# Kernel optimization log

Measured on AMD Instinct MI355X. Metric: run time of the kernel, lower is better.

The kernel has to match this reference:

```python
import jax, jax.numpy as jnp
import numpy as np

B, L, C = 2, 8192, 256
K, NLEV = 17, 4
HALF = K // 2


def setup_inputs() -> dict:
    key = jax.random.key(0)
    ks = jax.random.split(key, 10)
    s = 0.02
    return {
        "x": jax.random.normal(ks[0], (B, L, C), jnp.float32),
        "stem_w": jax.random.normal(ks[1], (C, C, 2), jnp.float32) * s,   # Conv1d (out,in,k)
        "stem_b": jax.random.normal(ks[2], (C,), jnp.float32) * s,
        "qkv_w": jax.random.normal(ks[3], (3 * C, C), jnp.float32) * s,
        "width_w": jax.random.normal(ks[4], (1, C), jnp.float32) * s,
        "width_b": jax.random.normal(ks[5], (1,), jnp.float32) * s,
        "out_w": jax.random.normal(ks[6], (C, C), jnp.float32) * s,
        "query": jax.random.normal(ks[7], (NLEV * C,), jnp.float32) * s,
        "film_w": jax.random.normal(ks[8], (2 * C, NLEV * C), jnp.float32) * s,
        "film_b": jax.random.normal(ks[9], (2 * C,), jnp.float32) * s,
    }


def _local_attn(h, qkv_w, width_w, width_b, out_w):
    # h: (b, l, c); 1D local windowed attention with learned sigmoid distance mask
    b, l, c = h.shape
    rel_dist = jnp.abs(jnp.arange(K, dtype=h.dtype) - HALF)  # (K,)
    max_dist = float(HALF)
    scale = c ** -0.5
    qkv = h @ qkv_w.T
    q, k, v = jnp.split(qkv, 3, axis=-1)
    width = jax.nn.sigmoid(h @ width_w.T + width_b) * max_dist + 0.5  # (b,l,1)
    k_pad = jnp.pad(k, ((0, 0), (HALF, HALF), (0, 0)))
    v_pad = jnp.pad(v, ((0, 0), (HALF, HALF), (0, 0)))
    idx = jnp.arange(l)[:, None] + jnp.arange(K)[None, :]  # (l,K) indices into padded seq
    k_win = k_pad[:, idx]  # (b,l,K,c)
    v_win = v_pad[:, idx]  # (b,l,K,c)
    scores = jnp.einsum('blc,blwc->blw', q, k_win) * scale
    soft_mask = jax.nn.sigmoid((width - rel_dist) * 5.0)  # (b,l,K)
    scores = scores - (1.0 - soft_mask) * 10000.0
    attn = jax.nn.softmax(scores, axis=-1)
    o = jnp.einsum('blw,blwc->blc', attn, v_win)
    return (o + v) @ out_w.T


def _forward(x, stem_w, stem_b, qkv_w, width_w, width_b, out_w, query, film_w, film_b):
    b, l, c = x.shape
    # stem conv: Conv1d(C, C, kernel=2, padding=1), then narrow to first l positions
    h = jnp.transpose(x, (0, 2, 1))  # (B,C,L)
    h = jax.lax.conv_general_dilated(h, stem_w, (1,), [(1, 1)],
                                     dimension_numbers=('NCH', 'OIH', 'NCH'))
    h = h[:, :, :l] + stem_b[None, :, None]
    h = jnp.transpose(h, (0, 2, 1))  # (B,L,C)
    levels = []
    for i in range(NLEV):
        h = _local_attn(h, qkv_w, width_w, width_b, out_w)
        levels.append(h)
        if i < NLEV - 1:  # avg_pool(kernel=2, stride=2)
            bl = h.shape[1]
            h = h.reshape(b, bl // 2, 2, c).mean(axis=2)
    # nearest upsample each coarser level back to L (factors are exact powers of 2)
    ups = [levels[0]]
    for lvl in levels[1:]:
        ups.append(jnp.repeat(lvl, l // lvl.shape[1], axis=1))
    concat = jnp.concatenate(ups, axis=-1)  # (B,L,NLEV*C)
    gattn = jax.nn.softmax(concat @ query, axis=-1)  # (B,L)
    global_ctx = jnp.einsum('bl,bld->bd', gattn, concat)  # (B,NLEV*C)
    film = global_ctx @ film_w.T + film_b  # (B,2C)
    scale_f, bias_f = jnp.split(film, 2, axis=-1)
    return levels[0] * (1.0 + scale_f[:, None, :]) + bias_f[:, None, :]


def reference(x, stem_w, stem_b, qkv_w, width_w, width_b, out_w, query, film_w, film_b):
    return _forward(x, stem_w, stem_b, qkv_w, width_w, width_b, out_w, query, film_w, film_b)
```

## Files before the change

### kernel.cpp

```cpp
#include <hip/hip_runtime.h>
#include <math.h>

#define L_SEQ 8192
#define B_SZ  2
#define CH    256
#define NLEV  4

typedef __attribute__((ext_vector_type(8))) short bf16x8;
typedef __attribute__((ext_vector_type(4))) float f32x4;

static __device__ __forceinline__ float sigmoidf_(float x) {
    return 1.0f / (1.0f + expf(-x));
}

static __device__ __forceinline__ float bf2f_(unsigned short u) {
    union { unsigned int ui; float f; } x;
    x.ui = ((unsigned int)u) << 16;
    return x.f;
}
static __device__ __forceinline__ unsigned short f2b_(float f) {
    union { float f; unsigned int u; } x;
    x.f = f;
    unsigned int lsb = (x.u >> 16) & 1u;
    unsigned int r = x.u + 0x7fffu + lsb;
    return (unsigned short)(r >> 16);
}
static __device__ __forceinline__ float4 ldb4_(const unsigned short* p) {
    ushort4 u = *(const ushort4*)p;
    return make_float4(bf2f_(u.x), bf2f_(u.y), bf2f_(u.z), bf2f_(u.w));
}

#define NPREP_BLOCKS 17409
__global__ __launch_bounds__(256) void prep_kernel(
    const float* __restrict__ x, const float* __restrict__ qkv_w,
    const float* __restrict__ out_w, const float* __restrict__ stem_w,
    unsigned short* __restrict__ x16g, unsigned short* __restrict__ qw16,
    unsigned short* __restrict__ sw16)
{
    __shared__ float owr[256];
    if (blockIdx.x >= NPREP_BLOCKS) {
        const int c = blockIdx.x - NPREP_BLOCKS, j = threadIdx.x;
        owr[j] = out_w[(size_t)c * 256 + j];
        __syncthreads();
        float acc = 0.0f;
        #pragma unroll 8
        for (int k = 0; k < 256; ++k)
            acc += owr[k] * qkv_w[(size_t)(512 + k) * 256 + j];
        qw16[(size_t)(512 + c) * 256 + j] = f2b_(acc);
        return;
    }
    int i = blockIdx.x * 256 + threadIdx.x;
    if (i < 256) { x16g[i] = 0; return; }
    i -= 256;
    if (i < 4194304) { x16g[256 + i] = f2b_(x[i]); return; }
    i -= 4194304;
    if (i < 131072) { qw16[i] = f2b_(qkv_w[i]); return; }
    i -= 131072;
    {
        int k = i & 511, nn = i >> 9;
        float v = (k < 256) ? stem_w[(size_t)nn * 512 + k * 2]
                            : stem_w[(size_t)nn * 512 + (k - 256) * 2 + 1];
        sw16[i] = f2b_(v);
    }
}

__global__ __launch_bounds__(256) void stem_gemm_bf16(
    const unsigned short* __restrict__ x16g, const unsigned short* __restrict__ W,
    unsigned short* __restrict__ outB, const float* __restrict__ bias)
{
    __shared__ unsigned short As[128 * 32];
    __shared__ unsigned short Bs[128 * 32];
    const int tid  = threadIdx.x;
    const int wave = tid >> 6;
    const int lane = tid & 63;
    const int bm = blockIdx.y * 128;
    const int bn = blockIdx.x * 128;
    const int wm = (wave & 1) * 64;
    const int wn = (wave >> 1) * 64;
    const int srow = lane >> 2;
    const int scol = (lane & 3) * 8;

    f32x4 acc[4][4] = {};

    for (int k0 = 0; k0 < 512; k0 += 32) {
        __syncthreads();
        #pragma unroll
        for (int c = 0; c < 2; ++c) {
            const int chunk = c * 4 + wave;
            const int row = bm + chunk * 16 + srow;
            const int t = row & (L_SEQ - 1);
            const unsigned short* ga;
            if (k0 < 256)
                ga = x16g + (t > 0 ? (size_t)row * 256 : 0) + k0 + scol;
            else
                ga = x16g + ((size_t)row + 1) * 256 + (k0 - 256) + scol;
            const unsigned short* gw = W + (size_t)(bn + chunk * 16 + srow) * 512 + k0 + scol;
            __builtin_amdgcn_global_load_lds(
                (const __attribute__((address_space(1))) void*)ga,
                (__attribute__((address_space(3))) void*)(As + chunk * 16 * 32),
                16, 0, 0);
            __builtin_amdgcn_global_load_lds(
                (const __attribute__((address_space(1))) void*)gw,
                (__attribute__((address_space(3))) void*)(Bs + chunk * 16 * 32),
                16, 0, 0);
        }
        __syncthreads();

        bf16x8 af[4], bf[4];
        const int fr = lane & 15;
        const int kk = (lane >> 4) * 8;
        #pragma unroll
        for (int i = 0; i < 4; ++i) {
            af[i] = *(const bf16x8*)(As + (wm + i * 16 + fr) * 32 + kk);
            bf[i] = *(const bf16x8*)(Bs + (wn + i * 16 + fr) * 32 + kk);
        }
        #pragma unroll
        for (int i = 0; i < 4; ++i)
            #pragma unroll
            for (int j = 0; j < 4; ++j)
                acc[i][j] = __builtin_amdgcn_mfma_f32_16x16x32_bf16(
                    af[i], bf[j], acc[i][j], 0, 0, 0);
    }

    const int cn = lane & 15;
    const int cr = (lane >> 4) * 4;
    #pragma unroll
    for (int i = 0; i < 4; ++i)
        #pragma unroll
        for (int r = 0; r < 4; ++r) {
            const int m = bm + wm + i * 16 + cr + r;
            #pragma unroll
            for (int j = 0; j < 4; ++j) {
                const int n = bn + wn + j * 16 + cn;
                outB[(size_t)m * CH + n] = f2b_(acc[i][j][r] + bias[n]);
            }
        }
}

__global__ __launch_bounds__(256) void gemm_bf16(
    const unsigned short* __restrict__ A, const unsigned short* __restrict__ W,
    unsigned short* __restrict__ outB, int M, int N, int Kd)
{
    __shared__ unsigned short As[128 * 32];
    __shared__ unsigned short Bs[128 * 32];
    const int tid  = threadIdx.x;
    const int wave = tid >> 6;
    const int lane = tid & 63;
    const int bm = blockIdx.y * 128;
    const int bn = blockIdx.x * 128;
    const int wm = (wave & 1) * 64;
    const int wn = (wave >> 1) * 64;
    const int srow = lane >> 2;
    const int scol = (lane & 3) * 8;

    f32x4 acc[4][4] = {};

    for (int k0 = 0; k0 < Kd; k0 += 32) {
        __syncthreads();
        #pragma unroll
        for (int c = 0; c < 2; ++c) {
            const int chunk = c * 4 + wave;
            const int row = chunk * 16 + srow;
            const unsigned short* ga = A + (size_t)(bm + row) * Kd + k0 + scol;
            const unsigned short* gw = W + (size_t)(bn + row) * Kd + k0 + scol;
            __builtin_amdgcn_global_load_lds(
                (const __attribute__((address_space(1))) void*)ga,
                (__attribute__((address_space(3))) void*)(As + chunk * 16 * 32),
                16, 0, 0);
            __builtin_amdgcn_global_load_lds(
                (const __attribute__((address_space(1))) void*)gw,
                (__attribute__((address_space(3))) void*)(Bs + chunk * 16 * 32),
                16, 0, 0);
        }
        __syncthreads();

        bf16x8 af[4], bf[4];
        const int fr = lane & 15;
        const int kk = (lane >> 4) * 8;
        #pragma unroll
        for (int i = 0; i < 4; ++i) {
            af[i] = *(const bf16x8*)(As + (wm + i * 16 + fr) * 32 + kk);
            bf[i] = *(const bf16x8*)(Bs + (wn + i * 16 + fr) * 32 + kk);
        }
        #pragma unroll
        for (int i = 0; i < 4; ++i)
            #pragma unroll
            for (int j = 0; j < 4; ++j)
                acc[i][j] = __builtin_amdgcn_mfma_f32_16x16x32_bf16(
                    af[i], bf[j], acc[i][j], 0, 0, 0);
    }

    const int cn = lane & 15;
    const int cr = (lane >> 4) * 4;
    #pragma unroll
    for (int i = 0; i < 4; ++i)
        #pragma unroll
        for (int r = 0; r < 4; ++r) {
            const int m = bm + wm + i * 16 + cr + r;
            const size_t rowoff = (size_t)m * N;
            #pragma unroll
            for (int j = 0; j < 4; ++j)
                outB[rowoff + bn + wn + j * 16 + cn] = f2b_(acc[i][j][r]);
        }
}

__global__ __launch_bounds__(512, 2) void attn_vp_kernel(
    const unsigned short* __restrict__ qkv, const unsigned short* __restrict__ h16,
    const float* __restrict__ ww, const float* __restrict__ wbp,
    unsigned short* __restrict__ l16o, unsigned short* __restrict__ dsB, int l)
{
    __shared__ __align__(16) unsigned short vt[256 * 88];
    __shared__ __align__(16) float sp1[4 * 2 * 64 * 4];
    __shared__ __align__(16) unsigned short pb[4 * 512];
    __shared__ float ws1[64];

    const int tid  = threadIdx.x;
    const int wave = tid >> 6;
    const int lane = tid & 63;
    const int rt   = wave & 3;
    const int half = wave >> 2;
    const int q    = lane >> 4;
    const int n    = lane & 15;

    int bid = blockIdx.x;
    const int cpx = gridDim.x >> 3;
    bid = (bid & 7) * cpx + (bid >> 3);

    const int bps = l >> 6;
    const int b  = bid / bps;
    const int t0 = (bid % bps) << 6;
    const size_t seqbase = (size_t)b * l;
    const int row0 = t0 + rt * 16;
    const int kc0  = half * 128;

    bf16x8 hv[4];
    {
        const unsigned short* hrow = h16 + (seqbase + row0 + n) * 256 + kc0 + q * 32;
        #pragma unroll
        for (int jj = 0; jj < 4; ++jj) hv[jj] = *(const bf16x8*)(hrow + jj * 8);
    }
    bf16x8 qf[4];
    {
        const unsigned short* qrow = qkv + (seqbase + row0 + n) * 768 + kc0 + q * 8;
        #pragma unroll
        for (int j = 0; j < 4; ++j) qf[j] = *(const bf16x8*)(qrow + j * 32);
    }
    bf16x8 bk[2][4];
    #pragma unroll
    for (int h = 0; h < 2; ++h) {
        const int grow = row0 - 8 + h * 16 + n;
        const bool ok = (grow >= 0 && grow < l);
        const unsigned short* kb = qkv + (seqbase + grow) * 768 + 256 + kc0 + q * 8;
        #pragma unroll
        for (int j = 0; j < 4; ++j) {
            bf16x8 z = {0, 0, 0, 0, 0, 0, 0, 0};
            bk[h][j] = ok ? *(const bf16x8*)(kb + j * 32) : z;
        }
    }
    bf16x8 vv[8];
    #pragma unroll
    for (int c = 0; c < 4; ++c)
        #pragma unroll
        for (int i = 0; i < 2; ++i) {
            const int r = i * 64 + lane;
            const int grow = t0 - 8 + r;
            bf16x8 val = {0, 0, 0, 0, 0, 0, 0, 0};
            if (r < 80 && grow >= 0 && grow < l)
                val = *(const bf16x8*)(qkv + (seqbase + grow) * 768 + 512 +
                                       (wave * 4 + c) * 8);
            vv[c * 2 + i] = val;
        }
    __builtin_amdgcn_sched_barrier(0);

    float wdot = 0.0f;
    #pragma unroll
    for (int jj = 0; jj < 4; ++jj) {
        float4 wa = *((const float4*)(ww + kc0 + q * 32 + jj * 8));
        float4 wc = *((const float4*)(ww + kc0 + q * 32 + jj * 8 + 4));
        wdot += bf2f_((unsigned short)hv[jj][0]) * wa.x
              + bf2f_((unsigned short)hv[jj][1]) * wa.y
              + bf2f_((unsigned short)hv[jj][2]) * wa.z
              + bf2f_((unsigned short)hv[jj][3]) * wa.w
              + bf2f_((unsigned short)hv[jj][4]) * wc.x
              + bf2f_((unsigned short)hv[jj][5]) * wc.y
              + bf2f_((unsigned short)hv[jj][6]) * wc.z
              + bf2f_((unsigned short)hv[jj][7]) * wc.w;
    }
    wdot += __shfl_xor(wdot, 16, 64);
    wdot += __shfl_xor(wdot, 32, 64);
    if (half == 1 && q == 0) ws1[rt * 16 + n] = wdot;

    f32x4 accS[2] = {};
    #pragma unroll
    for (int h = 0; h < 2; ++h)
        #pragma unroll
        for (int j = 0; j < 4; ++j)
            accS[h] = __builtin_amdgcn_mfma_f32_16x16x32_bf16(
                qf[j], bk[h][j], accS[h], 0, 0, 0);

    if (half == 1) {
        *(f32x4*)(sp1 + ((rt * 2 + 0) * 64 + lane) * 4) = accS[0];
        *(f32x4*)(sp1 + ((rt * 2 + 1) * 64 + lane) * 4) = accS[1];
    }

    #pragma unroll
    for (int c = 0; c < 4; ++c)
        #pragma unroll
        for (int i = 0; i < 2; ++i) {
            const int r = i * 64 + lane;
            if (i == 0 || lane < 16) {
                #pragma unroll
                for (int jj = 0; jj < 8; ++jj)
                    vt[((wave * 4 + c) * 8 + jj) * 88 + r] =
                        (unsigned short)vv[c * 2 + i][jj];
            }
        }

    __syncthreads();

    if (half == 0) {
        accS[0] += *(const f32x4*)(sp1 + ((rt * 2 + 0) * 64 + lane) * 4);
        accS[1] += *(const f32x4*)(sp1 + ((rt * 2 + 1) * 64 + lane) * 4);
        const float w_n = sigmoidf_(wdot + ws1[rt * 16 + n] + wbp[0]) * 8.0f + 0.5f;

        float wd[4];
        #pragma unroll
        for (int r = 0; r < 4; ++r) wd[r] = __shfl(w_n, q * 4 + r, 64);

        float s[2][4];
        #pragma unroll
        for (int h = 0; h < 2; ++h)
            #pragma unroll
            for (int r = 0; r < 4; ++r) {
                int ii = q * 4 + r;
                int c  = h * 16 + n;
                int w  = c - ii;
                float dist = fabsf((float)w - 8.0f);
                float sm = sigmoidf_((wd[r] - dist) * 5.0f);
                float v = accS[h][r] * 0.0625f - (1.0f - sm) * 10000.0f;
                s[h][r] = (w >= 0 && w <= 16) ? v : -3.0e38f;
            }

        float mx[4], sum[4];
        #pragma unroll
        for (int r = 0; r < 4; ++r) mx[r] = fmaxf(s[0][r], s[1][r]);
        #pragma unroll
        for (int m = 1; m < 16; m <<= 1)
            #pragma unroll
            for (int r = 0; r < 4; ++r) mx[r] = fmaxf(mx[r], __shfl_xor(mx[r], m, 64));
        float e[2][4];
        #pragma unroll
        for (int h = 0; h < 2; ++h)
            #pragma unroll
            for (int r = 0; r < 4; ++r) e[h][r] = expf(s[h][r] - mx[r]);
        #pragma unroll
        for (int r = 0; r < 4; ++r) sum[r] = e[0][r] + e[1][r];
        #pragma unroll
        for (int m = 1; m < 16; m <<= 1)
            #pragma unroll
            for (int r = 0; r < 4; ++r) sum[r] += __shfl_xor(sum[r], m, 64);

        #pragma unroll
        for (int h = 0; h < 2; ++h)
            #pragma unroll
            for (int r = 0; r < 4; ++r) {
                int ii = q * 4 + r, c = h * 16 + n;
                float p = e[h][r] / sum[r];
                if (c == ii + 8) p += 1.0f;
                pb[rt * 512 + ii * 32 + c] = f2b_(p);
            }
    }

    __syncthreads();

    bf16x8 pf = *(const bf16x8*)(pb + rt * 512 + n * 32 + q * 8);
    const int rl = q * 4;
    const size_t gbase = seqbase + row0;
    #pragma unroll
    for (int c = 0; c < 8; ++c) {
        const int ct = half * 8 + c;
        bf16x8 vf = *(const bf16x8*)(vt + (ct * 16 + n) * 88 + rt * 16 + q * 8);
        f32x4 z = {};
        f32x4 o = __builtin_amdgcn_mfma_f32_16x16x32_bf16(pf, vf, z, 0, 0, 0);
        const int col = ct * 16 + n;
        float v0 = o[0], v1 = o[1], v2 = o[2], v3 = o[3];
        size_t r0 = (gbase + rl) * CH + col;
        l16o[r0]          = f2b_(v0);
        l16o[r0 + CH]     = f2b_(v1);
        l16o[r0 + 2 * CH] = f2b_(v2);
        l16o[r0 + 3 * CH] = f2b_(v3);
        if (dsB) {
            size_t d0 = ((gbase + rl) >> 1) * CH + col;
            dsB[d0]      = f2b_(0.5f * (v0 + v1));
            dsB[d0 + CH] = f2b_(0.5f * (v2 + v3));
        }
    }
}

__global__ __launch_bounds__(1024) void tail_ctx_kernel(
    const unsigned short* __restrict__ l0, const unsigned short* __restrict__ l1,
    const unsigned short* __restrict__ l2, const unsigned short* __restrict__ l3,
    const float* __restrict__ query, float* __restrict__ partials,
    float* __restrict__ denomP)
{
    __shared__ float eS[128];
    const int tid = threadIdx.x;
    const int chunk = blockIdx.x, b = blockIdx.y;
    const int t0 = chunk * 128;
    const unsigned short* levp[4] = {l0, l1, l2, l3};

    const int w = tid >> 6, lane = tid & 63;
    const int lev = lane >> 4, c0 = (lane & 15) * 16;
    const unsigned short* lpbase = levp[lev] + (size_t)b * (L_SEQ >> lev) * CH;
    const float* qp = query + lev * CH + c0;
    float4 q0 = *(const float4*)(qp);
    float4 q1 = *(const float4*)(qp + 4);
    float4 q2 = *(const float4*)(qp + 8);
    float4 q3 = *(const float4*)(qp + 12);
    #pragma unroll
    for (int j = 0; j < 8; ++j) {
        int t = t0 + w * 8 + j;
        const unsigned short* p = lpbase + (size_t)(t >> lev) * CH + c0;
        float4 h0 = ldb4_(p), h1 = ldb4_(p + 4), h2 = ldb4_(p + 8), h3 = ldb4_(p + 12);
        float part = h0.x * q0.x + h0.y * q0.y + h0.z * q0.z + h0.w * q0.w
                   + h1.x * q1.x + h1.y * q1.y + h1.z * q1.z + h1.w * q1.w
                   + h2.x * q2.x + h2.y * q2.y + h2.z * q2.z + h2.w * q2.w
                   + h3.x * q3.x + h3.y * q3.y + h3.z * q3.z + h3.w * q3.w;
        #pragma unroll
        for (int m = 1; m < 64; m <<= 1) part += __shfl_xor(part, m, 64);
        if (lane == 0) eS[w * 8 + j] = expf(part);
    }
    __syncthreads();

    if (tid == 0) {
        float ds = 0.0f;
        #pragma unroll 8
        for (int i = 0; i < 128; ++i) ds += eS[i];
        denomP[b * 64 + chunk] = ds;
    }

    const int dlev = tid >> 8, c = tid & 255;
    const unsigned short* lp = levp[dlev] + (size_t)b * (L_SEQ >> dlev) * CH;
    float acc = 0.0f;
    #pragma unroll 4
    for (int t = t0; t < t0 + 128; ++t)
        acc += eS[t - t0] * bf2f_(lp[(size_t)(t >> dlev) * CH + c]);
    partials[(size_t)(b * 64 + chunk) * 1024 + tid] = acc;
}

__global__ __launch_bounds__(256) void ctx_reduce_kernel(
    const float* __restrict__ partials, const float* __restrict__ denomP,
    float* __restrict__ ctx)
{
    const int b = blockIdx.y;
    const int d = blockIdx.x * 256 + threadIdx.x;
    float acc = 0.0f;
    #pragma unroll
    for (int c = 0; c < 64; ++c) acc += partials[(size_t)(b * 64 + c) * 1024 + d];
    float den = 0.0f;
    #pragma unroll
    for (int c = 0; c < 64; ++c) den += denomP[b * 64 + c];
    ctx[b * 1024 + d] = acc / den;
}

__global__ __launch_bounds__(256) void film_kernel(
    const float* __restrict__ ctx, const float* __restrict__ fw,
    const float* __restrict__ fb, float* __restrict__ film)
{
    const int lane = threadIdx.x & 63;
    const int j = blockIdx.x * 4 + (threadIdx.x >> 6);
    float acc0 = 0.0f, acc1 = 0.0f;
    #pragma unroll
    for (int r = 0; r < 4; ++r) {
        float4 w4 = *((const float4*)(fw + (size_t)j * 1024 + r * 256) + lane);
        float4 c0 = *((const float4*)(ctx + r * 256) + lane);
        float4 c1 = *((const float4*)(ctx + 1024 + r * 256) + lane);
        acc0 += w4.x * c0.x + w4.y * c0.y + w4.z * c0.z + w4.w * c0.w;
        acc1 += w4.x * c1.x + w4.y * c1.y + w4.z * c1.z + w4.w * c1.w;
    }
    #pragma unroll
    for (int m = 1; m < 64; m <<= 1) {
        acc0 += __shfl_xor(acc0, m, 64);
        acc1 += __shfl_xor(acc1, m, 64);
    }
    if (lane == 0) {
        float b = fb[j];
        film[j] = acc0 + b;
        film[512 + j] = acc1 + b;
    }
}

__global__ void final_kernel(const unsigned short* __restrict__ lev0,
                             const float* __restrict__ film,
                             float* __restrict__ out)
{
    size_t n4 = ((size_t)blockIdx.x * 256 + threadIdx.x) * 4;
    int c = (int)(n4 & (CH - 1));
    int b = (int)(n4 >> 21);
    float4 h = ldb4_(lev0 + n4);
    const float* fs = film + b * 512;
    float4 o;
    o.x = h.x * (1.0f + fs[c + 0]) + fs[256 + c + 0];
    o.y = h.y * (1.0f + fs[c + 1]) + fs[256 + c + 1];
    o.z = h.z * (1.0f + fs[c + 2]) + fs[256 + c + 2];
    o.w = h.w * (1.0f + fs[c + 3]) + fs[256 + c + 3];
    *(float4*)(out + n4) = o;
}

extern "C" void kernel_launch(void* const* d_in, const int* in_sizes, int n_in,
                              void* d_out, int out_size, void* d_ws, size_t ws_size,
                              hipStream_t stream) {
    const float* x       = (const float*)d_in[0];
    const float* stem_w  = (const float*)d_in[1];
    const float* stem_b  = (const float*)d_in[2];
    const float* qkv_w   = (const float*)d_in[3];
    const float* width_w = (const float*)d_in[4];
    const float* width_b = (const float*)d_in[5];
    const float* out_w   = (const float*)d_in[6];
    const float* query   = (const float*)d_in[7];
    const float* film_w  = (const float*)d_in[8];
    const float* film_b  = (const float*)d_in[9];
    float* out = (float*)d_out;
    float* ws  = (float*)d_ws;

    float* partials = ws;
    float* denomP   = partials + 131072;
    float* ctx      = denomP + 128;
    float* film     = ctx + 2048;
    unsigned short* x16g  = (unsigned short*)(film + 1024);
    unsigned short* h16_0 = x16g + 4194560;
    unsigned short* h16_1 = h16_0 + 4194304;
    unsigned short* h16_2 = h16_1 + 2097152;
    unsigned short* h16_3 = h16_2 + 1048576;
    unsigned short* qkv16 = h16_3 + 524288;
    unsigned short* ov16  = qkv16 + 12582912;
    unsigned short* l16_0 = ov16 + 4194304;
    unsigned short* l16_1 = l16_0 + 4194304;
    unsigned short* l16_2 = l16_1 + 2097152;
    unsigned short* l16_3 = l16_2 + 1048576;
    unsigned short* qw16  = l16_3 + 524288;
    unsigned short* ow16  = qw16 + 196608;
    unsigned short* sw16  = ow16 + 65536;
    unsigned short* h16[4]  = {h16_0, h16_1, h16_2, h16_3};
    unsigned short* l16[4]  = {l16_0, l16_1, l16_2, l16_3};
    (void)ov16; (void)ow16;

    prep_kernel<<<NPREP_BLOCKS + 256, 256, 0, stream>>>(
        x, qkv_w, out_w, stem_w, x16g, qw16, sw16);

    stem_gemm_bf16<<<dim3(CH / 128, B_SZ * L_SEQ / 128), 256, 0, stream>>>(
        x16g, sw16, h16_0, stem_b);

    for (int i = 0; i < NLEV; ++i) {
        const int l = L_SEQ >> i;
        const int M = B_SZ * l;
        gemm_bf16<<<dim3(768 / 128, M / 128), 256, 0, stream>>>(
            h16[i], qw16, qkv16, M, 768, CH);
        attn_vp_kernel<<<M / 64, 512, 0, stream>>>(
            qkv16, h16[i], width_w, width_b,
            l16[i], (i < NLEV - 1) ? h16[i + 1] : nullptr, l);
    }

    tail_ctx_kernel<<<dim3(64, B_SZ), 1024, 0, stream>>>(
        l16_0, l16_1, l16_2, l16_3, query, partials, denomP);
    ctx_reduce_kernel<<<dim3(4, B_SZ), 256, 0, stream>>>(partials, denomP, ctx);
    film_kernel<<<128, 256, 0, stream>>>(ctx, film_w, film_b, film);
    final_kernel<<<(B_SZ * L_SEQ * CH) / 1024, 256, 0, stream>>>(l16_0, film, out);
}
```

Before: 241.3 us.

## Fuse QKV projection GEMM into the per-level local attention kernel

```diff
diff --git a/kernel.cpp b/kernel.cpp
--- a/kernel.cpp
+++ b/kernel.cpp
@@ -137,82 +137,20 @@
         }
 }
 
-__global__ __launch_bounds__(256) void gemm_bf16(
-    const unsigned short* __restrict__ A, const unsigned short* __restrict__ W,
-    unsigned short* __restrict__ outB, int M, int N, int Kd)
-{
-    __shared__ unsigned short As[128 * 32];
-    __shared__ unsigned short Bs[128 * 32];
-    const int tid  = threadIdx.x;
-    const int wave = tid >> 6;
-    const int lane = tid & 63;
-    const int bm = blockIdx.y * 128;
-    const int bn = blockIdx.x * 128;
-    const int wm = (wave & 1) * 64;
-    const int wn = (wave >> 1) * 64;
-    const int srow = lane >> 2;
-    const int scol = (lane & 3) * 8;
-
-    f32x4 acc[4][4] = {};
-
-    for (int k0 = 0; k0 < Kd; k0 += 32) {
-        __syncthreads();
-        #pragma unroll
-        for (int c = 0; c < 2; ++c) {
-            const int chunk = c * 4 + wave;
-            const int row = chunk * 16 + srow;
-            const unsigned short* ga = A + (size_t)(bm + row) * Kd + k0 + scol;
-            const unsigned short* gw = W + (size_t)(bn + row) * Kd + k0 + scol;
-            __builtin_amdgcn_global_load_lds(
-                (const __attribute__((address_space(1))) void*)ga,
-                (__attribute__((address_space(3))) void*)(As + chunk * 16 * 32),
-                16, 0, 0);
-            __builtin_amdgcn_global_load_lds(
-                (const __attribute__((address_space(1))) void*)gw,
-                (__attribute__((address_space(3))) void*)(Bs + chunk * 16 * 32),
-                16, 0, 0);
-        }
-        __syncthreads();
-
-        bf16x8 af[4], bf[4];
-        const int fr = lane & 15;
-        const int kk = (lane >> 4) * 8;
-        #pragma unroll
-        for (int i = 0; i < 4; ++i) {
-            af[i] = *(const bf16x8*)(As + (wm + i * 16 + fr) * 32 + kk);
-            bf[i] = *(const bf16x8*)(Bs + (wn + i * 16 + fr) * 32 + kk);
-        }
-        #pragma unroll
-        for (int i = 0; i < 4; ++i)
-            #pragma unroll
-            for (int j = 0; j < 4; ++j)
-                acc[i][j] = __builtin_amdgcn_mfma_f32_16x16x32_bf16(
-                    af[i], bf[j], acc[i][j], 0, 0, 0);
-    }
-
-    const int cn = lane & 15;
-    const int cr = (lane >> 4) * 4;
-    #pragma unroll
-    for (int i = 0; i < 4; ++i)
-        #pragma unroll
-        for (int r = 0; r < 4; ++r) {
-            const int m = bm + wm + i * 16 + cr + r;
-            const size_t rowoff = (size_t)m * N;
-            #pragma unroll
-            for (int j = 0; j < 4; ++j)
-                outB[rowoff + bn + wn + j * 16 + cn] = f2b_(acc[i][j][r]);
-        }
-}
-
-__global__ __launch_bounds__(512, 2) void attn_vp_kernel(
-    const unsigned short* __restrict__ qkv, const unsigned short* __restrict__ h16,
+__global__ __launch_bounds__(512, 2) void level_fused_kernel(
+    const unsigned short* __restrict__ h16in, const unsigned short* __restrict__ qw,
+    const unsigned short* __restrict__ zrow,
     const float* __restrict__ ww, const float* __restrict__ wbp,
     unsigned short* __restrict__ l16o, unsigned short* __restrict__ dsB, int l)
 {
-    __shared__ __align__(16) unsigned short vt[256 * 88];
-    __shared__ __align__(16) float sp1[4 * 2 * 64 * 4];
-    __shared__ __align__(16) unsigned short pb[4 * 512];
-    __shared__ float ws1[64];
+    __shared__ __align__(16) char smem[127232];
+    unsigned short* hs = (unsigned short*)smem;
+    unsigned short* qs = (unsigned short*)(smem + 40960);
+    unsigned short* ks = (unsigned short*)(smem + 73728);
+    unsigned short* vt = (unsigned short*)(smem + 40960);
+    unsigned short* pb = (unsigned short*)(smem + 114688);
+    float* sp1 = (float*)(smem + 118784);
+    float* ws1 = (float*)(smem + 126976);
 
     const int tid  = threadIdx.x;
     const int wave = tid >> 6;
@@ -231,91 +169,147 @@
     const int t0 = (bid % bps) << 6;
     const size_t seqbase = (size_t)b * l;
     const int row0 = t0 + rt * 16;
-    const int kc0  = half * 128;
-
-    bf16x8 hv[4];
+
+    #pragma unroll
+    for (int i = 0; i < 5; ++i) {
+        const int task = i * 512 + tid;
+        const int r = task >> 5, ch = task & 31;
+        const int grow = t0 - 8 + r;
+        const unsigned short* src = (grow >= 0 && grow < l)
+            ? h16in + (seqbase + grow) * 256 + ((ch ^ (r & 7)) << 3)
+            : zrow;
+        __builtin_amdgcn_global_load_lds(
+            (const __attribute__((address_space(1))) void*)src,
+            (__attribute__((address_space(3))) void*)
+                (hs + (size_t)(i * 512 + (tid & ~63)) * 8),
+            16, 0, 0);
+    }
+    __syncthreads();
+
+    const int ct0 = wave * 2;
     {
-        const unsigned short* hrow = h16 + (seqbase + row0 + n) * 256 + kc0 + q * 32;
-        #pragma unroll
-        for (int jj = 0; jj < 4; ++jj) hv[jj] = *(const bf16x8*)(hrow + jj * 8);
-    }
-    bf16x8 qf[4];
+        bf16x8 bwa[8], bwb[8];
+        const unsigned short* wa_ = qw + (size_t)(ct0 * 16 + n) * 256 + q * 8;
+        const unsigned short* wb_ = qw + (size_t)((ct0 + 1) * 16 + n) * 256 + q * 8;
+        #pragma unroll
+        for (int j = 0; j < 8; ++j) {
+            bwa[j] = *(const bf16x8*)(wa_ + j * 32);
+            bwb[j] = *(const bf16x8*)(wb_ + j * 32);
+        }
+        #pragma unroll
+        for (int rtq = 0; rtq < 4; ++rtq) {
+            const int hr = 8 + rtq * 16 + n;
+            const int hswz = (hr & 7) << 4;
+            bf16x8 af[8];
+            #pragma unroll
+            for (int j = 0; j < 8; ++j)
+                af[j] = *(const bf16x8*)((const char*)hs +
+                         ((hr * 512 + (j * 32 + q * 8) * 2) ^ hswz));
+            f32x4 aA = {}, aB = {};
+            #pragma unroll
+            for (int j = 0; j < 8; ++j) {
+                aA = __builtin_amdgcn_mfma_f32_16x16x32_bf16(af[j], bwa[j], aA, 0, 0, 0);
+                aB = __builtin_amdgcn_mfma_f32_16x16x32_bf16(af[j], bwb[j], aB, 0, 0, 0);
+            }
+            #pragma unroll
+            for (int idx = 0; idx < 4; ++idx) {
+                const int row = rtq * 16 + q * 4 + idx;
+                const int rswz = (row & 7) << 4;
+                *(unsigned short*)((char*)qs +
+                    ((row * 512 + (ct0 * 16 + n) * 2) ^ rswz)) = f2b_(aA[idx]);
+                *(unsigned short*)((char*)qs +
+                    ((row * 512 + ((ct0 + 1) * 16 + n) * 2) ^ rswz)) = f2b_(aB[idx]);
+            }
+        }
+    }
     {
-        const unsigned short* qrow = qkv + (seqbase + row0 + n) * 768 + kc0 + q * 8;
-        #pragma unroll
-        for (int j = 0; j < 4; ++j) qf[j] = *(const bf16x8*)(qrow + j * 32);
-    }
-    bf16x8 bk[2][4];
-    #pragma unroll
-    for (int h = 0; h < 2; ++h) {
-        const int grow = row0 - 8 + h * 16 + n;
-        const bool ok = (grow >= 0 && grow < l);
-        const unsigned short* kb = qkv + (seqbase + grow) * 768 + 256 + kc0 + q * 8;
-        #pragma unroll
-        for (int j = 0; j < 4; ++j) {
-            bf16x8 z = {0, 0, 0, 0, 0, 0, 0, 0};
-            bk[h][j] = ok ? *(const bf16x8*)(kb + j * 32) : z;
-        }
-    }
-    bf16x8 vv[8];
-    #pragma unroll
-    for (int c = 0; c < 4; ++c)
-        #pragma unroll
-        for (int i = 0; i < 2; ++i) {
-            const int r = i * 64 + lane;
-            const int grow = t0 - 8 + r;
-            bf16x8 val = {0, 0, 0, 0, 0, 0, 0, 0};
-            if (r < 80 && grow >= 0 && grow < l)
-                val = *(const bf16x8*)(qkv + (seqbase + grow) * 768 + 512 +
-                                       (wave * 4 + c) * 8);
-            vv[c * 2 + i] = val;
-        }
-    __builtin_amdgcn_sched_barrier(0);
-
+        bf16x8 bwa[8], bwb[8];
+        const unsigned short* wa_ = qw + (size_t)(256 + ct0 * 16 + n) * 256 + q * 8;
+        const unsigned short* wb_ = qw + (size_t)(256 + (ct0 + 1) * 16 + n) * 256 + q * 8;
+        #pragma unroll
+        for (int j = 0; j < 8; ++j) {
+            bwa[j] = *(const bf16x8*)(wa_ + j * 32);
+            bwb[j] = *(const bf16x8*)(wb_ + j * 32);
+        }
+        #pragma unroll
+        for (int rtk = 0; rtk < 5; ++rtk) {
+            const int hr = rtk * 16 + n;
+            const int hswz = (hr & 7) << 4;
+            bf16x8 af[8];
+            #pragma unroll
+            for (int j = 0; j < 8; ++j)
+                af[j] = *(const bf16x8*)((const char*)hs +
+                         ((hr * 512 + (j * 32 + q * 8) * 2) ^ hswz));
+            f32x4 aA = {}, aB = {};
+            #pragma unroll
+            for (int j = 0; j < 8; ++j) {
+                aA = __builtin_amdgcn_mfma_f32_16x16x32_bf16(af[j], bwa[j], aA, 0, 0, 0);
+                aB = __builtin_amdgcn_mfma_f32_16x16x32_bf16(af[j], bwb[j], aB, 0, 0, 0);
+            }
+            #pragma unroll
+            for (int idx = 0; idx < 4; ++idx) {
+                const int row = rtk * 16 + q * 4 + idx;
+                const int rswz = (row & 7) << 4;
+                *(unsigned short*)((char*)ks +
+                    ((row * 512 + (ct0 * 16 + n) * 2) ^ rswz)) = f2b_(aA[idx]);
+                *(unsigned short*)((char*)ks +
+                    ((row * 512 + ((ct0 + 1) * 16 + n) * 2) ^ rswz)) = f2b_(aB[idx]);
+            }
+        }
+    }
+    __syncthreads();
+
+    const int kc0 = half * 128;
     float wdot = 0.0f;
-    #pragma unroll
-    for (int jj = 0; jj < 4; ++jj) {
-        float4 wa = *((const float4*)(ww + kc0 + q * 32 + jj * 8));
-        float4 wc = *((const float4*)(ww + kc0 + q * 32 + jj * 8 + 4));
-        wdot += bf2f_((unsigned short)hv[jj][0]) * wa.x
-              + bf2f_((unsigned short)hv[jj][1]) * wa.y
-              + bf2f_((unsigned short)hv[jj][2]) * wa.z
-              + bf2f_((unsigned short)hv[jj][3]) * wa.w
-              + bf2f_((unsigned short)hv[jj][4]) * wc.x
-              + bf2f_((unsigned short)hv[jj][5]) * wc.y
-              + bf2f_((unsigned short)hv[jj][6]) * wc.z
-              + bf2f_((unsigned short)hv[jj][7]) * wc.w;
+    {
+        const int hr = 8 + rt * 16 + n;
+        const int hswz = (hr & 7) << 4;
+        #pragma unroll
+        for (int jj = 0; jj < 4; ++jj) {
+            bf16x8 hv = *(const bf16x8*)((const char*)hs +
+                        ((hr * 512 + (kc0 + q * 32 + jj * 8) * 2) ^ hswz));
+            float4 wa = *((const float4*)(ww + kc0 + q * 32 + jj * 8));
+            float4 wc = *((const float4*)(ww + kc0 + q * 32 + jj * 8 + 4));
+            wdot += bf2f_((unsigned short)hv[0]) * wa.x
+                  + bf2f_((unsigned short)hv[1]) * wa.y
+                  + bf2f_((unsigned short)hv[2]) * wa.z
+                  + bf2f_((unsigned short)hv[3]) * wa.w
+                  + bf2f_((unsigned short)hv[4]) * wc.x
+                  + bf2f_((unsigned short)hv[5]) * wc.y
+                  + bf2f_((unsigned short)hv[6]) * wc.z
+                  + bf2f_((unsigned short)hv[7]) * wc.w;
+        }
     }
     wdot += __shfl_xor(wdot, 16, 64);
     wdot += __shfl_xor(wdot, 32, 64);
     if (half == 1 && q == 0) ws1[rt * 16 + n] = wdot;
 
     f32x4 accS[2] = {};
-    #pragma unroll
-    for (int h = 0; h < 2; ++h)
+    {
+        const int qrow = rt * 16 + n;
+        const int qswz = (qrow & 7) << 4;
+        bf16x8 qf[4];
         #pragma unroll
         for (int j = 0; j < 4; ++j)
-            accS[h] = __builtin_amdgcn_mfma_f32_16x16x32_bf16(
-                qf[j], bk[h][j], accS[h], 0, 0, 0);
-
+            qf[j] = *(const bf16x8*)((const char*)qs +
+                     ((qrow * 512 + (kc0 + q * 8 + j * 32) * 2) ^ qswz));
+        #pragma unroll
+        for (int h = 0; h < 2; ++h) {
+            const int rk = rt * 16 + h * 16 + n;
+            const int kswz = (rk & 7) << 4;
+            #pragma unroll
+            for (int j = 0; j < 4; ++j) {
+                bf16x8 kb = *(const bf16x8*)((const char*)ks +
+                            ((rk * 512 + (kc0 + q * 8 + j * 32) * 2) ^ kswz));
+                accS[h] = __builtin_amdgcn_mfma_f32_16x16x32_bf16(
+                    qf[j], kb, accS[h], 0, 0, 0);
+            }
+        }
+    }
     if (half == 1) {
         *(f32x4*)(sp1 + ((rt * 2 + 0) * 64 + lane) * 4) = accS[0];
         *(f32x4*)(sp1 + ((rt * 2 + 1) * 64 + lane) * 4) = accS[1];
     }
-
-    #pragma unroll
-    for (int c = 0; c < 4; ++c)
-        #pragma unroll
-        for (int i = 0; i < 2; ++i) {
-            const int r = i * 64 + lane;
-            if (i == 0 || lane < 16) {
-                #pragma unroll
-                for (int jj = 0; jj < 8; ++jj)
-                    vt[((wave * 4 + c) * 8 + jj) * 88 + r] =
-                        (unsigned short)vv[c * 2 + i][jj];
-            }
-        }
-
     __syncthreads();
 
     if (half == 0) {
@@ -370,7 +364,40 @@
                 pb[rt * 512 + ii * 32 + c] = f2b_(p);
             }
     }
-
+    __syncthreads();
+
+    {
+        bf16x8 bwa[8], bwb[8];
+        const unsigned short* wa_ = qw + (size_t)(512 + ct0 * 16 + n) * 256 + q * 8;
+        const unsigned short* wb_ = qw + (size_t)(512 + (ct0 + 1) * 16 + n) * 256 + q * 8;
+        #pragma unroll
+        for (int j = 0; j < 8; ++j) {
+            bwa[j] = *(const bf16x8*)(wa_ + j * 32);
+            bwb[j] = *(const bf16x8*)(wb_ + j * 32);
+        }
+        #pragma unroll
+        for (int rtv = 0; rtv < 5; ++rtv) {
+            const int hr = rtv * 16 + n;
+            const int hswz = (hr & 7) << 4;
+            bf16x8 af[8];
+            #pragma unroll
+            for (int j = 0; j < 8; ++j)
+                af[j] = *(const bf16x8*)((const char*)hs +
+                         ((hr * 512 + (j * 32 + q * 8) * 2) ^ hswz));
+            f32x4 aA = {}, aB = {};
+            #pragma unroll
+            for (int j = 0; j < 8; ++j) {
+                aA = __builtin_amdgcn_mfma_f32_16x16x32_bf16(af[j], bwa[j], aA, 0, 0, 0);
+                aB = __builtin_amdgcn_mfma_f32_16x16x32_bf16(af[j], bwb[j], aB, 0, 0, 0);
+            }
+            ushort4 pA, pB;
+            pA.x = f2b_(aA[0]); pA.y = f2b_(aA[1]); pA.z = f2b_(aA[2]); pA.w = f2b_(aA[3]);
+            pB.x = f2b_(aB[0]); pB.y = f2b_(aB[1]); pB.z = f2b_(aB[2]); pB.w = f2b_(aB[3]);
+            const int rb = rtv * 16 + q * 4;
+            *(ushort4*)(vt + (size_t)(ct0 * 16 + n) * 88 + rb) = pA;
+            *(ushort4*)(vt + (size_t)((ct0 + 1) * 16 + n) * 88 + rb) = pB;
+        }
+    }
     __syncthreads();
 
     bf16x8 pf = *(const bf16x8*)(pb + rt * 512 + n * 32 + q * 8);
@@ -543,7 +570,7 @@
     unsigned short* sw16  = ow16 + 65536;
     unsigned short* h16[4]  = {h16_0, h16_1, h16_2, h16_3};
     unsigned short* l16[4]  = {l16_0, l16_1, l16_2, l16_3};
-    (void)ov16; (void)ow16;
+    (void)qkv16; (void)ov16; (void)ow16;
 
     prep_kernel<<<NPREP_BLOCKS + 256, 256, 0, stream>>>(
         x, qkv_w, out_w, stem_w, x16g, qw16, sw16);
@@ -554,10 +581,8 @@
     for (int i = 0; i < NLEV; ++i) {
         const int l = L_SEQ >> i;
         const int M = B_SZ * l;
-        gemm_bf16<<<dim3(768 / 128, M / 128), 256, 0, stream>>>(
-            h16[i], qw16, qkv16, M, 768, CH);
-        attn_vp_kernel<<<M / 64, 512, 0, stream>>>(
-            qkv16, h16[i], width_w, width_b,
+        level_fused_kernel<<<M / 64, 512, 0, stream>>>(
+            h16[i], qw16, x16g , width_w, width_b,
             l16[i], (i < NLEV - 1) ? h16[i + 1] : nullptr, l);
     }
 
```

After: 227.0 us. 1.06x faster.
